# Optimization experiments

Hardware: AMD Instinct MI355X
Metric: run time of the kernel (lower is better)

Reference implementation:

```python
import jax, jax.numpy as jnp
import numpy as np
from jax import lax

B, H, W = 16, 96, 320
NUM_JOINTS = 9
THRESH = 0.1


def _nms(heat):
    # 3x3 max-pool NMS: keep only local maxima
    hmax = lax.reduce_window(heat, -jnp.inf, lax.max, (1, 1, 3, 3), (1, 1, 1, 1), 'SAME')
    return jnp.where(hmax == heat, heat, jnp.zeros_like(heat))


def _gather_feat(feat_bhc, ind):
    # feat_bhc: (B, HW, C), ind: (B, K) -> (B, K, C)
    return jnp.take_along_axis(feat_bhc, ind[:, :, None], axis=1)


def _transpose_and_gather_feat(feat, ind):
    # feat: (B, C, H, W), ind: (B, K) -> (B, K, C)
    b, c = feat.shape[0], feat.shape[1]
    f = feat.reshape(b, c, -1).transpose(0, 2, 1)  # (B, HW, C)
    return _gather_feat(f, ind)


def _topk(heat, K):
    b, c, h, w = heat.shape
    scores = heat.reshape(b, c, h * w)
    topk_scores, topk_inds = lax.top_k(scores, K)            # (B, C, K)
    topk_ys = (topk_inds // w).astype(heat.dtype)
    topk_xs = (topk_inds % w).astype(heat.dtype)
    topk_score, topk_ind = lax.top_k(topk_scores.reshape(b, c * K), K)  # (B, K)
    clses = topk_ind // K
    g = lambda a: jnp.take_along_axis(a.reshape(b, c * K), topk_ind, axis=1)
    return topk_score, g(topk_inds), clses, g(topk_ys), g(topk_xs)


def _topk_channel(heat, K):
    b, c, h, w = heat.shape
    scores = heat.reshape(b, c, h * w)
    topk_scores, topk_inds = lax.top_k(scores, K)  # (B, C, K)
    topk_ys = (topk_inds // w).astype(heat.dtype)
    topk_xs = (topk_inds % w).astype(heat.dtype)
    return topk_scores, topk_inds, topk_ys, topk_xs


def setup_inputs() -> dict:
    key = jax.random.key(0)
    ks = jax.random.split(key, 9)
    mk = lambda k, c: jax.random.normal(k, (B, c, H, W), dtype=jnp.float32)
    return {
        'hm': mk(ks[0], 3), 'wh': mk(ks[1], 2), 'hps': mk(ks[2], 18),
        'dim': mk(ks[3], 3), 'rot': mk(ks[4], 8), 'prob': mk(ks[5], 1),
        'reg': mk(ks[6], 2), 'hm_hp': mk(ks[7], 9), 'hp_offset': mk(ks[8], 2),
        'K': 100,
    }


def _decode(hm, wh, hps, dim, rot, prob, reg, hm_hp, hp_offset, K):
    b = hm.shape[0]
    J = hps.shape[1] // 2
    heat = _nms(jax.nn.sigmoid(hm))
    scores, inds, clses, ys0, xs0 = _topk(heat, K)  # (B, K) each

    kps = _transpose_and_gather_feat(hps, inds).reshape(b, K, J, 2)
    kps = kps + jnp.stack([xs0, ys0], axis=-1)[:, :, None, :]  # add center coords

    reg_g = _transpose_and_gather_feat(reg, inds)  # (B, K, 2)
    xs = xs0[:, :, None] + reg_g[:, :, 0:1]
    ys = ys0[:, :, None] + reg_g[:, :, 1:2]

    wh_g = _transpose_and_gather_feat(wh, inds)  # (B, K, 2)
    clses_f = clses.astype(hm.dtype)[:, :, None]
    scores_f = scores[:, :, None]
    bboxes = jnp.concatenate([xs - wh_g[..., 0:1] / 2, ys - wh_g[..., 1:2] / 2,
                              xs + wh_g[..., 0:1] / 2, ys + wh_g[..., 1:2] / 2], axis=2)

    dim_g = _transpose_and_gather_feat(dim, inds)        # (B, K, 3)
    rot_g = _transpose_and_gather_feat(rot, inds)        # (B, K, 8)
    prob_g = _transpose_and_gather_feat(prob, inds)[:, :, 0:1]  # (B, K, 1)

    # keypoint heatmap refinement
    hmhp = _nms(jax.nn.sigmoid(hm_hp))
    kps_jk = kps.transpose(0, 2, 1, 3)  # (B, J, K, 2)
    hm_score, hm_inds, hm_ys, hm_xs = _topk_channel(hmhp, K)  # (B, J, K)
    hp_off = _transpose_and_gather_feat(hp_offset, hm_inds.reshape(b, -1)).reshape(b, J, K, 2)
    hm_xs = hm_xs + hp_off[..., 0]
    hm_ys = hm_ys + hp_off[..., 1]

    valid = hm_score > THRESH
    hm_score = jnp.where(valid, hm_score, -1.0)
    hm_ys = jnp.where(valid, hm_ys, -10000.0)
    hm_xs = jnp.where(valid, hm_xs, -10000.0)
    hm_kps = jnp.stack([hm_xs, hm_ys], axis=-1)  # (B, J, K, 2)

    dist = jnp.sqrt(((kps_jk[:, :, :, None, :] - hm_kps[:, :, None, :, :]) ** 2).sum(-1))  # (B,J,K,K)
    min_dist = dist.min(axis=3)
    min_ind = dist.argmin(axis=3)  # (B, J, K)
    hm_score_sel = jnp.take_along_axis(hm_score, min_ind, axis=2)[..., None]  # (B,J,K,1)
    hm_kps_sel = jnp.take_along_axis(hm_kps, min_ind[..., None], axis=2)      # (B,J,K,2)

    l = bboxes[:, :, 0][:, None, :, None]
    t = bboxes[:, :, 1][:, None, :, None]
    r = bboxes[:, :, 2][:, None, :, None]
    bb = bboxes[:, :, 3][:, None, :, None]
    md = min_dist[..., None]
    invalid = ((hm_kps_sel[..., 0:1] < l) | (hm_kps_sel[..., 0:1] > r) |
               (hm_kps_sel[..., 1:2] < t) | (hm_kps_sel[..., 1:2] > bb) |
               (hm_score_sel < THRESH) | (md > jnp.maximum(bb - t, r - l) * 0.3))
    kps_out = jnp.where(invalid, kps_jk, hm_kps_sel)  # (B, J, K, 2)
    kps_final = kps_out.transpose(0, 2, 1, 3).reshape(b, K, J * 2) * 4.0
    hm_score_out = hm_score_sel[..., 0].transpose(0, 2, 1)  # (B, K, J)

    bboxes = bboxes * 4.0
    detections = jnp.concatenate(
        [bboxes, scores_f, kps_final, dim_g, hm_score_out, rot_g, prob_g, clses_f], axis=2)
    return detections  # (B, K, 4+1+18+3+9+8+1+1 = 45)


def reference(hm, wh, hps, dim, rot, prob, reg, hm_hp, hp_offset, K):
    return _decode(hm, wh, hps, dim, rot, prob, reg, hm_hp, hp_offset, K)
```

## Files before the change

kernel.cpp:

```cpp
#include <hip/hip_runtime.h>
#include <math.h>

typedef unsigned int u32;
typedef unsigned short u16;
typedef unsigned long long u64;

#define HW    30720
#define W_    320
#define H_    96
#define B_    16
#define KTOP  100
#define NIMG  192
#define NTHR  1024
#define SCAP  4096

__global__ __launch_bounds__(NTHR) void fused_nms_select_kernel(
    const float* __restrict__ hm, const float* __restrict__ hm_hp,
    u32* __restrict__ tkKey, u32* __restrict__ tkIdx)
{
    const int row = blockIdx.x;
    const int tid = threadIdx.x;

    __shared__ __align__(16) float img[HW];
    __shared__ u32 candKey[SCAP];
    __shared__ u16 candPix[SCAP];
    __shared__ u32 chunkv[256];
    __shared__ u32 selb1, cnt, cnt2;

    u32* hist  = (u32*)img;
    u64* cand2 = (u64*)(img + 4096);

    if (tid == 0) { cnt = 0; cnt2 = 0; }

    const float4* src4 = (const float4*)((row < 48)
        ? (hm + (size_t)row * HW) : (hm_hp + (size_t)(row - 48) * HW));
    float4* img4 = (float4*)img;
    #pragma unroll
    for (int j = 0; j < 8; ++j) {
        int i = tid + j * NTHR;
        if (i < HW / 4) img4[i] = src4[i];
    }
    __syncthreads();

    for (int q = tid; q < HW / 4; q += NTHR) {
        int pix0 = q * 4;
        int y = pix0 / W_;
        int x0 = pix0 - y * W_;
        int ym = (y > 0 ? y - 1 : 0) * W_;
        int yc = y * W_;
        int yp = (y < H_ - 1 ? y + 1 : H_ - 1) * W_;
        float cm[6];
        #pragma unroll
        for (int c = 0; c < 6; ++c) {
            int xc = x0 - 1 + c;
            xc = (xc < 0) ? 0 : (xc > W_ - 1 ? W_ - 1 : xc);
            cm[c] = fmaxf(fmaxf(img[ym + xc], img[yc + xc]), img[yp + xc]);
        }
        #pragma unroll
        for (int j = 0; j < 4; ++j) {
            float cen = img[yc + x0 + j];
            float m = fmaxf(fmaxf(cm[j], cm[j + 1]), cm[j + 2]);
            if (cen == m) {
                float s = 1.0f / (1.0f + expf(-cen));
                u32 p = atomicAdd(&cnt, 1u);
                if (p < SCAP) {
                    candKey[p] = __float_as_uint(s);
                    candPix[p] = (u16)(pix0 + j);
                }
            }
        }
    }
    __syncthreads();
    const u32 n = (cnt > SCAP) ? SCAP : cnt;

    #pragma unroll
    for (int j = 0; j < 4; ++j) hist[tid + j * NTHR] = 0;
    __syncthreads();
    for (u32 i = tid; i < n; i += NTHR)
        atomicAdd(&hist[candKey[i] >> 20], 1u);
    __syncthreads();
    if (tid < 256) {
        u32 s = 0; int c0 = tid * 16;
        #pragma unroll
        for (int q = 0; q < 16; ++q) s += hist[c0 + q];
        chunkv[tid] = s;
    }
    __syncthreads();
    for (int d = 1; d < 256; d <<= 1) {
        u32 t = 0;
        if (tid < 256 - d) t = chunkv[tid + d];
        __syncthreads();
        if (tid < 256) chunkv[tid] += t;
        __syncthreads();
    }
    if (tid < 256) {
        u32 Sc = chunkv[tid];
        u32 Sn = (tid == 255) ? 0u : chunkv[tid + 1];
        if (Sc >= KTOP && Sn < KTOP) {
            u32 run = Sn;
            for (int bin = tid * 16 + 15; bin >= tid * 16; --bin) {
                u32 h = hist[bin];
                if (run + h >= KTOP) { selb1 = (u32)bin; break; }
                run += h;
            }
        }
    }
    __syncthreads();
    const u32 b1 = selb1;

    for (u32 i = tid; i < n; i += NTHR) {
        u32 k = candKey[i];
        if ((k >> 20) >= b1) {
            u32 p = atomicAdd(&cnt2, 1u);
            if (p < 2048) cand2[p] = ((u64)k << 32) | (u32)(~(u32)candPix[i]);
        }
    }
    __syncthreads();
    u32 q = cnt2; if (q > 2048) q = 2048;

    if (q <= NTHR) {
        if (tid < q) {
            u64 v = cand2[tid];
            u32 rank = 0;
            for (u32 i = 0; i < q; ++i) rank += (cand2[i] > v);
            if (rank < KTOP) {
                tkKey[row * KTOP + rank] = (u32)(v >> 32);
                tkIdx[row * KTOP + rank] = ~(u32)v;
            }
        }
    } else {
        u32 npow = 128; while (npow < q) npow <<= 1;
        for (u32 i = q + tid; i < npow; i += NTHR) cand2[i] = 0ull;
        __syncthreads();
        for (u32 ks = 2; ks <= npow; ks <<= 1) {
            for (u32 j = ks >> 1; j > 0; j >>= 1) {
                for (u32 i = tid; i < npow; i += NTHR) {
                    u32 ix = i ^ j;
                    if (ix > i) {
                        u64 a = cand2[i], b = cand2[ix];
                        bool sw = ((i & ks) == 0) ? (a < b) : (a > b);
                        if (sw) { cand2[i] = b; cand2[ix] = a; }
                    }
                }
                __syncthreads();
            }
        }
        if (tid < KTOP) {
            u64 v = cand2[tid];
            tkKey[row * KTOP + tid] = (u32)(v >> 32);
            tkIdx[row * KTOP + tid] = ~(u32)v;
        }
    }
}

__global__ __launch_bounds__(320) void decode_kernel(
    const u32* __restrict__ tkKey, const u32* __restrict__ tkIdx,
    const float* __restrict__ wh,   const float* __restrict__ hps,
    const float* __restrict__ dimp, const float* __restrict__ rot,
    const float* __restrict__ prob, const float* __restrict__ reg,
    const float* __restrict__ hpo,  float* __restrict__ det)
{
    const int blk = blockIdx.x;
    const int b = blk / 9;
    const int j = blk - b * 9;
    const int tid = threadIdx.x;

    __shared__ u64 arr[300];
    __shared__ u64 selv[KTOP];
    __shared__ float hsv[KTOP], hxv[KTOP], hyv[KTOP];

    if (tid < 300) {
        int c = tid / 100, r = tid - c * 100;
        u32 key = tkKey[(b * 3 + c) * KTOP + r];
        arr[tid] = ((u64)key << 32) | (u32)(~(u32)tid);
    }
    __syncthreads();
    if (tid < 300) {
        u64 v = arr[tid];
        u32 rank = 0;
        for (int i = 0; i < 300; ++i) rank += (arr[i] > v);
        if (rank < KTOP) selv[rank] = v;
    }
    __syncthreads();

    float l = 0.f, t = 0.f, rr = 0.f, bb = 0.f, kxr = 0.f, kyr = 0.f;

    if (tid < KTOP) {
        int k = tid;
        u64 v = selv[k];
        u32 pos = ~(u32)v;
        if (pos > 299u) pos = 299u;
        u32 key = (u32)(v >> 32);
        int c = (int)pos / 100, r = (int)pos - c * 100;
        u32 sid = tkIdx[(b * 3 + c) * KTOP + r];
        if (sid > HW - 1) sid = HW - 1;
        float score = __uint_as_float(key);
        int yy = (int)sid / W_, xx = (int)sid - yy * W_;
        float xs0 = (float)xx, ys0 = (float)yy;
        float r0 = reg[((size_t)b * 2 + 0) * HW + sid];
        float r1 = reg[((size_t)b * 2 + 1) * HW + sid];
        float xsv = xs0 + r0, ysv = ys0 + r1;
        float w0 = wh[((size_t)b * 2 + 0) * HW + sid];
        float w1 = wh[((size_t)b * 2 + 1) * HW + sid];
        l  = xsv - w0 * 0.5f;
        t  = ysv - w1 * 0.5f;
        rr = xsv + w0 * 0.5f;
        bb = ysv + w1 * 0.5f;
        kxr = hps[((size_t)b * 18 + 2 * j)     * HW + sid] + xs0;
        kyr = hps[((size_t)b * 18 + 2 * j + 1) * HW + sid] + ys0;
        if (j == 0) {
            float* o = det + ((size_t)b * KTOP + k) * 45;
            o[0] = l * 4.0f; o[1] = t * 4.0f; o[2] = rr * 4.0f; o[3] = bb * 4.0f;
            o[4] = score;
            o[44] = (float)c;
        }
    } else if (tid < 200) {
        int r = tid - 100;
        int rw = 48 + b * 9 + j;
        u32 key = tkKey[rw * KTOP + r];
        u32 idx = tkIdx[rw * KTOP + r];
        if (idx > HW - 1) idx = HW - 1;
        float s = __uint_as_float(key);
        int yy = (int)idx / W_, xx = (int)idx - yy * W_;
        float hx = (float)xx + hpo[((size_t)b * 2 + 0) * HW + idx];
        float hy = (float)yy + hpo[((size_t)b * 2 + 1) * HW + idx];
        bool valid = s > 0.1f;
        hsv[r] = valid ? s : -1.0f;
        hxv[r] = valid ? hx : -10000.0f;
        hyv[r] = valid ? hy : -10000.0f;
    } else if (tid < 300 && j == 0) {
        int k = tid - 200;
        u64 v = selv[k];
        u32 pos = ~(u32)v;
        if (pos > 299u) pos = 299u;
        int c = (int)pos / 100, r = (int)pos - c * 100;
        u32 sid = tkIdx[(b * 3 + c) * KTOP + r];
        if (sid > HW - 1) sid = HW - 1;
        float* o = det + ((size_t)b * KTOP + k) * 45;
        #pragma unroll
        for (int qq = 0; qq < 3; ++qq)
            o[23 + qq] = dimp[((size_t)b * 3 + qq) * HW + sid];
        #pragma unroll
        for (int qq = 0; qq < 8; ++qq)
            o[35 + qq] = rot[((size_t)b * 8 + qq) * HW + sid];
        o[43] = prob[(size_t)b * HW + sid];
    }
    __syncthreads();

    if (tid < KTOP) {
        int k = tid;
        float best = INFINITY; int bi = 0;
        for (int m = 0; m < 100; ++m) {
            float dx = kxr - hxv[m];
            float dy = kyr - hyv[m];
            float d2 = __fadd_rn(__fmul_rn(dx, dx), __fmul_rn(dy, dy));
            float d = __fsqrt_rn(d2);
            if (d < best) { best = d; bi = m; }
        }
        float ss = hsv[bi], hx = hxv[bi], hy = hyv[bi];
        float th = __fmul_rn(fmaxf(__fsub_rn(bb, t), __fsub_rn(rr, l)), 0.3f);
        bool invalid = (hx < l) | (hx > rr) | (hy < t) | (hy > bb) |
                       (ss < 0.1f) | (best > th);
        float ox = invalid ? kxr : hx;
        float oy = invalid ? kyr : hy;
        float* o = det + ((size_t)b * KTOP + k) * 45;
        o[5 + 2 * j] = ox * 4.0f;
        o[6 + 2 * j] = oy * 4.0f;
        o[26 + j]    = ss;
    }
}

extern "C" void kernel_launch(void* const* d_in, const int* in_sizes, int n_in,
                              void* d_out, int out_size, void* d_ws, size_t ws_size,
                              hipStream_t stream) {
    const float* hm    = (const float*)d_in[0];
    const float* wh    = (const float*)d_in[1];
    const float* hps   = (const float*)d_in[2];
    const float* dimp  = (const float*)d_in[3];
    const float* rot   = (const float*)d_in[4];
    const float* prob  = (const float*)d_in[5];
    const float* reg   = (const float*)d_in[6];
    const float* hm_hp = (const float*)d_in[7];
    const float* hpo   = (const float*)d_in[8];
    float* det = (float*)d_out;

    u32* tkKey = (u32*)d_ws;
    u32* tkIdx = tkKey + NIMG * KTOP;

    fused_nms_select_kernel<<<NIMG, NTHR, 0, stream>>>(hm, hm_hp, tkKey, tkIdx);
    decode_kernel<<<B_ * 9, 320, 0, stream>>>(tkKey, tkIdx, wh, hps, dimp, rot,
                                              prob, reg, hpo, det);
}
```

Baseline: 163.8 us.

## Read NMS neighborhood from global memory and add two-level radix threshold select

Drops the 120KB shared-memory staging of each heatmap image and reads the 3x3 neighborhood straight from global memory with float4 loads plus scalar halo loads. This cuts LDS use, which may allow more blocks per CU, at the cost of redundant global/L2 reads. The histogram scan is replaced by a single-wavefront shuffle scan, and a second 12-bit histogram level refines the cutoff so fewer candidates reach the final ranking.

```diff
diff --git a/kernel.cpp b/kernel.cpp
--- a/kernel.cpp
+++ b/kernel.cpp
@@ -21,96 +21,152 @@
     const int row = blockIdx.x;
     const int tid = threadIdx.x;
 
-    __shared__ __align__(16) float img[HW];
     __shared__ u32 candKey[SCAP];
     __shared__ u16 candPix[SCAP];
-    __shared__ u32 chunkv[256];
-    __shared__ u32 selb1, cnt, cnt2;
-
-    u32* hist  = (u32*)img;
-    u64* cand2 = (u64*)(img + 4096);
+    __shared__ u32 hist[4096];
+    __shared__ u32 selb1, selG1, selb2;
+    __shared__ u32 cnt, cnt2;
+
+    u64* cand2 = (u64*)hist;
 
     if (tid == 0) { cnt = 0; cnt2 = 0; }
-
-    const float4* src4 = (const float4*)((row < 48)
-        ? (hm + (size_t)row * HW) : (hm_hp + (size_t)(row - 48) * HW));
-    float4* img4 = (float4*)img;
     #pragma unroll
-    for (int j = 0; j < 8; ++j) {
-        int i = tid + j * NTHR;
-        if (i < HW / 4) img4[i] = src4[i];
-    }
+    for (int j = 0; j < 4; ++j) hist[tid + j * NTHR] = 0;
+
+    const float* __restrict__ base = (row < 48)
+        ? (hm + (size_t)row * HW) : (hm_hp + (size_t)(row - 48) * HW);
     __syncthreads();
 
     for (int q = tid; q < HW / 4; q += NTHR) {
-        int pix0 = q * 4;
-        int y = pix0 / W_;
-        int x0 = pix0 - y * W_;
-        int ym = (y > 0 ? y - 1 : 0) * W_;
-        int yc = y * W_;
-        int yp = (y < H_ - 1 ? y + 1 : H_ - 1) * W_;
-        float cm[6];
-        #pragma unroll
-        for (int c = 0; c < 6; ++c) {
-            int xc = x0 - 1 + c;
-            xc = (xc < 0) ? 0 : (xc > W_ - 1 ? W_ - 1 : xc);
-            cm[c] = fmaxf(fmaxf(img[ym + xc], img[yc + xc]), img[yp + xc]);
-        }
+        int y  = q / 80;
+        int qx = q - y * 80;
+        int x0 = qx * 4;
+        const float* rm = base + (y > 0 ? y - 1 : 0) * W_;
+        const float* rc = base + y * W_;
+        const float* rp = base + (y < H_ - 1 ? y + 1 : H_ - 1) * W_;
+        float4 am = *(const float4*)(rm + x0);
+        float4 ac = *(const float4*)(rc + x0);
+        float4 ap = *(const float4*)(rp + x0);
+        float cm0 = fmaxf(fmaxf(am.x, ac.x), ap.x);
+        float cm1 = fmaxf(fmaxf(am.y, ac.y), ap.y);
+        float cm2 = fmaxf(fmaxf(am.z, ac.z), ap.z);
+        float cm3 = fmaxf(fmaxf(am.w, ac.w), ap.w);
+        float cl, cr;
+        if (qx > 0)
+            cl = fmaxf(fmaxf(rm[x0 - 1], rc[x0 - 1]), rp[x0 - 1]);
+        else cl = cm0;
+        if (qx < 79)
+            cr = fmaxf(fmaxf(rm[x0 + 4], rc[x0 + 4]), rp[x0 + 4]);
+        else cr = cm3;
+
+        float cen[4] = {ac.x, ac.y, ac.z, ac.w};
+        float mx[4];
+        mx[0] = fmaxf(fmaxf(cl,  cm0), cm1);
+        mx[1] = fmaxf(fmaxf(cm0, cm1), cm2);
+        mx[2] = fmaxf(fmaxf(cm1, cm2), cm3);
+        mx[3] = fmaxf(fmaxf(cm2, cm3), cr);
         #pragma unroll
         for (int j = 0; j < 4; ++j) {
-            float cen = img[yc + x0 + j];
-            float m = fmaxf(fmaxf(cm[j], cm[j + 1]), cm[j + 2]);
-            if (cen == m) {
-                float s = 1.0f / (1.0f + expf(-cen));
+            if (cen[j] == mx[j]) {
+                float s = 1.0f / (1.0f + expf(-cen[j]));
                 u32 p = atomicAdd(&cnt, 1u);
                 if (p < SCAP) {
                     candKey[p] = __float_as_uint(s);
-                    candPix[p] = (u16)(pix0 + j);
+                    candPix[p] = (u16)(x0 + j + y * W_);
                 }
             }
         }
     }
     __syncthreads();
     const u32 n = (cnt > SCAP) ? SCAP : cnt;
+
+    for (u32 i = tid; i < n; i += NTHR)
+        atomicAdd(&hist[candKey[i] >> 20], 1u);
+    __syncthreads();
+    if (tid < 64) {
+        int lane = tid;
+        u32 v[4], t[4];
+        #pragma unroll
+        for (int k = 0; k < 4; ++k) {
+            u32 s = 0; int b0 = (lane * 4 + k) * 16;
+            #pragma unroll
+            for (int qq = 0; qq < 16; ++qq) s += hist[b0 + qq];
+            v[k] = s;
+        }
+        t[3] = v[3]; t[2] = v[2] + t[3]; t[1] = v[1] + t[2]; t[0] = v[0] + t[1];
+        u32 lt = t[0], s = lt;
+        #pragma unroll
+        for (int d = 1; d < 64; d <<= 1) {
+            u32 o = __shfl_down(s, d);
+            if (lane + d < 64) s += o;
+        }
+        u32 SH = s - lt;
+        u32 sfx[5] = {t[0] + SH, t[1] + SH, t[2] + SH, t[3] + SH, SH};
+        #pragma unroll
+        for (int k = 0; k < 4; ++k) {
+            if (sfx[k] >= KTOP && sfx[k + 1] < KTOP) {
+                u32 run = sfx[k + 1];
+                int c = lane * 4 + k;
+                for (int bin = c * 16 + 15; bin >= c * 16; --bin) {
+                    u32 h = hist[bin];
+                    if (run + h >= KTOP) { selb1 = (u32)bin; selG1 = run; break; }
+                    run += h;
+                }
+            }
+        }
+    }
+    __syncthreads();
+    const u32 b1 = selb1, G1 = selG1;
 
     #pragma unroll
     for (int j = 0; j < 4; ++j) hist[tid + j * NTHR] = 0;
     __syncthreads();
-    for (u32 i = tid; i < n; i += NTHR)
-        atomicAdd(&hist[candKey[i] >> 20], 1u);
-    __syncthreads();
-    if (tid < 256) {
-        u32 s = 0; int c0 = tid * 16;
-        #pragma unroll
-        for (int q = 0; q < 16; ++q) s += hist[c0 + q];
-        chunkv[tid] = s;
-    }
-    __syncthreads();
-    for (int d = 1; d < 256; d <<= 1) {
-        u32 t = 0;
-        if (tid < 256 - d) t = chunkv[tid + d];
-        __syncthreads();
-        if (tid < 256) chunkv[tid] += t;
-        __syncthreads();
-    }
-    if (tid < 256) {
-        u32 Sc = chunkv[tid];
-        u32 Sn = (tid == 255) ? 0u : chunkv[tid + 1];
-        if (Sc >= KTOP && Sn < KTOP) {
-            u32 run = Sn;
-            for (int bin = tid * 16 + 15; bin >= tid * 16; --bin) {
-                u32 h = hist[bin];
-                if (run + h >= KTOP) { selb1 = (u32)bin; break; }
-                run += h;
-            }
-        }
-    }
-    __syncthreads();
-    const u32 b1 = selb1;
-
     for (u32 i = tid; i < n; i += NTHR) {
         u32 k = candKey[i];
-        if ((k >> 20) >= b1) {
+        if ((k >> 20) == b1) atomicAdd(&hist[(k >> 8) & 0xFFFu], 1u);
+    }
+    __syncthreads();
+    {
+        const u32 K2 = KTOP - G1;
+        if (tid < 64) {
+            int lane = tid;
+            u32 v[4], t[4];
+            #pragma unroll
+            for (int k = 0; k < 4; ++k) {
+                u32 s = 0; int b0 = (lane * 4 + k) * 16;
+                #pragma unroll
+                for (int qq = 0; qq < 16; ++qq) s += hist[b0 + qq];
+                v[k] = s;
+            }
+            t[3] = v[3]; t[2] = v[2] + t[3]; t[1] = v[1] + t[2]; t[0] = v[0] + t[1];
+            u32 lt = t[0], s = lt;
+            #pragma unroll
+            for (int d = 1; d < 64; d <<= 1) {
+                u32 o = __shfl_down(s, d);
+                if (lane + d < 64) s += o;
+            }
+            u32 SH = s - lt;
+            u32 sfx[5] = {t[0] + SH, t[1] + SH, t[2] + SH, t[3] + SH, SH};
+            #pragma unroll
+            for (int k = 0; k < 4; ++k) {
+                if (sfx[k] >= K2 && sfx[k + 1] < K2) {
+                    u32 run = sfx[k + 1];
+                    int c = lane * 4 + k;
+                    for (int bin = c * 16 + 15; bin >= c * 16; --bin) {
+                        u32 h = hist[bin];
+                        if (run + h >= K2) { selb2 = (u32)bin; break; }
+                        run += h;
+                    }
+                }
+            }
+        }
+    }
+    __syncthreads();
+    const u32 cut24 = (b1 << 12) | selb2;
+
+    for (u32 i = tid; i < n; i += NTHR) {
+        u32 k = candKey[i];
+        if ((k >> 8) >= cut24) {
             u32 p = atomicAdd(&cnt2, 1u);
             if (p < 2048) cand2[p] = ((u64)k << 32) | (u32)(~(u32)candPix[i]);
         }
```

Result: faster. 156.6 us (-4.4%).
